# Kernel tuning notes

Measured on AMD Instinct MI355X. Metric: run time of the kernel, lower is better.

The kernel has to match this reference:

```python
import jax, jax.numpy as jnp
import numpy as np

B, N, L, K = 32, 512, 8, 8


def setup_inputs() -> dict:
    key = jax.random.key(0)
    k1, k2 = jax.random.split(key)
    A = jax.random.normal(k1, (B, N, N), dtype=jnp.float32)
    A = 0.5 * (A + A.transpose(0, 2, 1))  # symmetric matrix, as in MMF use-case
    O_stack = jax.random.normal(k2, (L, B, K, K), dtype=jnp.float32)  # per-level KxK rotations
    rng = np.random.default_rng(0)
    idx = np.stack([np.sort(rng.choice(N, K, replace=False)) for _ in range(B * L)])
    indices = jnp.asarray(idx.reshape(B, L, K), dtype=jnp.int32)  # sorted, distinct per (b,l)
    wavelet = indices[:, :, 0]  # wavelet index is one of the selected indices per level
    return {"A": A, "O_stack": O_stack, "indices": indices, "wavelet": wavelet}


def reference(A, O_stack, indices, wavelet):
    Bz, Nz, _ = A.shape
    Lz = O_stack.shape[0]
    eye = jnp.eye(Nz, dtype=A.dtype)

    def build_U(idx, O):
        # identity except the KxK block at (idx_i, idx_j) replaced by O
        # (matches torch boolean-mask row-major fill since idx is sorted)
        return eye.at[idx[:, None], idx[None, :]].set(O)

    right = None
    for l in range(Lz):
        U = jax.vmap(build_U)(indices[:, l], O_stack[l])  # [B,N,N]
        right = U if l == 0 else U @ right
        A = U @ A @ U.transpose(0, 2, 1)

    # final masking: zero rows/cols of wavelet indices, keep diagonal
    active = jnp.ones((Bz, Nz), dtype=A.dtype).at[jnp.arange(Bz)[:, None], wavelet].set(0.0)
    left = active[:, :, None] * active[:, None, :]
    d = jnp.arange(Nz)
    left = left.at[:, d, d].set(1.0)
    D = A * left
    A_rec = right.transpose(0, 2, 1) @ D @ right
    return (A_rec, right, D)
```

## Files before the change

### kernel.cpp

```cpp
#include <hip/hip_runtime.h>

#define BATCH 32
#define NDIM 512
#define LNUM 8
#define KDIM 8

#define WS_PM     0
#define WS_S      512
#define WS_ACT    640
#define WS_W      1152
#define WS_B2     5248
#define WS_C2     9344
#define WS_RA     13440
#define WS_RD     46208
#define WS_RAT    78976
#define WS_RDT    111744
#define WS_STRIDE 144512

#define LSTR 65
typedef float f4 __attribute__((ext_vector_type(4)));

__global__ __launch_bounds__(256) void k_small(
    const float* __restrict__ A, const float* __restrict__ O,
    const int* __restrict__ indices, const int* __restrict__ wavelet,
    float* __restrict__ ws)
{
    const int b = blockIdx.x;
    const int tid = threadIdx.x;
    float* base = ws + (size_t)b * WS_STRIDE;

    __shared__ float Wl[64*LSTR];
    __shared__ float P1[64*LSTR];
    __shared__ float P2[64*LSTR];
    __shared__ float B2l[64*LSTR];
    __shared__ int   pml[NDIM];
    __shared__ float actl[NDIM];
    __shared__ float actS[64];
    __shared__ int   idxsh[64];
    __shared__ int   Ssh[64];
    __shared__ int   prow[KDIM];
    __shared__ float Oall[LNUM*KDIM*KDIM];
    __shared__ int   s_sh;

    for (int t = tid; t < LNUM*KDIM*KDIM; t += 256) {
        int l = t >> 6, k = t & 63;
        Oall[t] = O[((size_t)l*BATCH + b)*(KDIM*KDIM) + k];
    }
    if (tid < 64) idxsh[tid] = indices[b*64 + tid];
    for (int n = tid; n < NDIM; n += 256) { pml[n] = -1; actl[n] = 1.f; }
    __syncthreads();

    if (tid < 64) {
        int n = idxsh[tid];
        bool first = true;
        for (int t = 0; t < tid; ++t) if (idxsh[t] == n) first = false;
        unsigned long long m = __ballot(first);
        int rank = __popcll(m & ((1ull << tid) - 1ull));
        if (first) { pml[n] = rank; Ssh[rank] = n; }
        if (tid == 0) s_sh = (int)__popcll(m);
    }
    if (tid >= 64 && tid < 64 + LNUM) {
        actl[wavelet[b*LNUM + (tid - 64)]] = 0.f;
    }
    __syncthreads();
    const int s = s_sh;
    if (tid < 64 && tid >= s) Ssh[tid] = 0;
    __syncthreads();
    if (tid < 64) actS[tid] = actl[Ssh[tid]];

    {
        int*   g_posmap = (int*)(base + WS_PM);
        int*   g_S      = (int*)(base + WS_S);
        float* g_act    = base + WS_ACT;
        for (int n = tid; n < NDIM; n += 256) { g_posmap[n] = pml[n]; g_act[n] = actl[n]; }
        if (tid < 64) g_S[tid] = Ssh[tid];
    }

    for (int t = tid; t < 4096; t += 256) {
        int rr = t >> 6, cc = t & 63;
        Wl[rr*LSTR + cc] = (rr == cc && rr < s) ? 1.f : 0.f;
    }
    __syncthreads();
    for (int l = 0; l < LNUM; ++l) {
        if (tid < KDIM) prow[tid] = pml[idxsh[l*KDIM + tid]];
        __syncthreads();
        for (int t = tid; t < KDIM*64; t += 256) {
            int i = t >> 6, c = t & 63;
            float acc = 0.f;
            #pragma unroll
            for (int j = 0; j < KDIM; ++j)
                acc += Oall[l*64 + i*KDIM + j] * Wl[prow[j]*LSTR + c];
            B2l[t] = acc;
        }
        __syncthreads();
        for (int t = tid; t < KDIM*64; t += 256) {
            int i = t >> 6, c = t & 63;
            Wl[prow[i]*LSTR + c] = B2l[t];
        }
        __syncthreads();
    }
    {
        float* g_W = base + WS_W;
        for (int t = tid; t < 4096; t += 256) g_W[t] = Wl[(t>>6)*LSTR + (t&63)];
    }

    for (int t = tid; t < 4096; t += 256) {
        int n = t >> 6, m = t & 63;
        P1[n*LSTR + m] = A[((size_t)b*NDIM + Ssh[n])*NDIM + Ssh[m]];
    }
    __syncthreads();

    const int w = tid >> 6;
    const int ln = tid & 63;
    float acc[16];

    #pragma unroll
    for (int k = 0; k < 16; ++k) acc[k] = 0.f;
    for (int n = 0; n < 64; ++n) {
        float as = P1[n*LSTR + ln];
        #pragma unroll
        for (int k = 0; k < 16; ++k) acc[k] += Wl[(w*16 + k)*LSTR + n] * as;
    }
    #pragma unroll
    for (int k = 0; k < 16; ++k) P2[(w*16 + k)*LSTR + ln] = acc[k];
    __syncthreads();

    #pragma unroll
    for (int k = 0; k < 16; ++k) acc[k] = 0.f;
    for (int m = 0; m < 64; ++m) {
        float wv = Wl[ln*LSTR + m];
        #pragma unroll
        for (int k = 0; k < 16; ++k) acc[k] += P2[(w*16 + k)*LSTR + m] * wv;
    }
    #pragma unroll
    for (int k = 0; k < 16; ++k) B2l[(w*16 + k)*LSTR + ln] = acc[k];
    __syncthreads();
    {
        float* g_B2 = base + WS_B2;
        for (int t = tid; t < 4096; t += 256) g_B2[t] = B2l[(t>>6)*LSTR + (t&63)];
    }

    for (int t = tid; t < 4096; t += 256) {
        int n = t >> 6, m = t & 63;
        float mv = (Ssh[n] == Ssh[m]) ? 1.f : actS[n]*actS[m];
        P1[n*LSTR + m] = mv * B2l[n*LSTR + m];
    }
    __syncthreads();

    #pragma unroll
    for (int k = 0; k < 16; ++k) acc[k] = 0.f;
    for (int n = 0; n < 64; ++n) {
        float dv = P1[n*LSTR + ln];
        #pragma unroll
        for (int k = 0; k < 16; ++k) acc[k] += Wl[n*LSTR + (w*16 + k)] * dv;
    }
    #pragma unroll
    for (int k = 0; k < 16; ++k) P2[(w*16 + k)*LSTR + ln] = acc[k];
    __syncthreads();

    #pragma unroll
    for (int k = 0; k < 16; ++k) acc[k] = 0.f;
    for (int m = 0; m < 64; ++m) {
        float wv = Wl[m*LSTR + ln];
        #pragma unroll
        for (int k = 0; k < 16; ++k) acc[k] += P2[(w*16 + k)*LSTR + m] * wv;
    }
    {
        float* g_C2 = base + WS_C2;
        #pragma unroll
        for (int k = 0; k < 16; ++k) g_C2[(w*16 + k)*64 + ln] = acc[k];
    }
}

__global__ __launch_bounds__(256) void k_mid(const float* __restrict__ A,
                                             float* __restrict__ ws)
{
    const int b = blockIdx.x;
    const int j0 = blockIdx.y * 64;
    const int tid = threadIdx.x;
    float* base = ws + (size_t)b * WS_STRIDE;
    const int*   g_S   = (const int*)(base + WS_S);
    const float* g_act = base + WS_ACT;
    const float* g_W   = base + WS_W;
    float* g_RA  = base + WS_RA;
    float* g_RD  = base + WS_RD;
    float* g_RAT = base + WS_RAT;
    float* g_RDT = base + WS_RDT;

    __shared__ float Wl[64*LSTR];
    __shared__ float AS[64*64];
    __shared__ float RAt[64*64];
    __shared__ int   Ssh[64];
    __shared__ float actS[64];
    __shared__ float actj[64];

    for (int t = tid; t < 1024; t += 256) {
        f4 w = ((const f4*)g_W)[t];
        int r = t >> 4, c = (t & 15) * 4;
        Wl[r*LSTR + c]   = w.x; Wl[r*LSTR + c+1] = w.y;
        Wl[r*LSTR + c+2] = w.z; Wl[r*LSTR + c+3] = w.w;
    }
    if (tid < 64) {
        int n = g_S[tid];
        Ssh[tid] = n;
        actS[tid] = g_act[n];
    }
    if (tid >= 64 && tid < 128) actj[tid-64] = g_act[j0 + (tid-64)];
    __syncthreads();

    for (int t = tid; t < 1024; t += 256) {
        int n = t >> 4, cc = (t & 15) * 4;
        f4 v = ((const f4*)(A + ((size_t)b*NDIM + Ssh[n])*NDIM + j0))[t & 15];
        AS[n*64 + cc]   = v.x; AS[n*64 + cc+1] = v.y;
        AS[n*64 + cc+2] = v.z; AS[n*64 + cc+3] = v.w;
    }
    __syncthreads();

    const int g = tid >> 6;
    const int j = tid & 63;
    float racc[16];

    #pragma unroll
    for (int k = 0; k < 16; ++k) racc[k] = 0.f;
    for (int n = 0; n < 64; ++n) {
        float av = AS[n*64 + j];
        #pragma unroll
        for (int k = 0; k < 16; ++k) racc[k] += Wl[(g*16 + k)*LSTR + n] * av;
    }
    #pragma unroll
    for (int k = 0; k < 16; ++k) {
        RAt[(g*16 + k)*64 + j] = racc[k];
        g_RA[(g*16 + k)*NDIM + j0 + j] = racc[k];
    }
    {
        f4* dst = (f4*)(g_RAT + (size_t)(j0 + j)*64 + g*16);
        #pragma unroll
        for (int q = 0; q < 4; ++q) {
            f4 v = { racc[4*q], racc[4*q+1], racc[4*q+2], racc[4*q+3] };
            dst[q] = v;
        }
    }
    __syncthreads();

    #pragma unroll
    for (int k = 0; k < 16; ++k) racc[k] = 0.f;
    for (int n = 0; n < 64; ++n) {
        float dt = actS[n] * RAt[n*64 + j];
        #pragma unroll
        for (int k = 0; k < 16; ++k) racc[k] += Wl[n*LSTR + g*16 + k] * dt;
    }
    const float aj = actj[j];
    #pragma unroll
    for (int k = 0; k < 16; ++k) {
        float rd = racc[k] * aj;
        racc[k] = rd;
        g_RD[(g*16 + k)*NDIM + j0 + j] = rd;
    }
    {
        f4* dst = (f4*)(g_RDT + (size_t)(j0 + j)*64 + g*16);
        #pragma unroll
        for (int q = 0; q < 4; ++q) {
            f4 v = { racc[4*q], racc[4*q+1], racc[4*q+2], racc[4*q+3] };
            dst[q] = v;
        }
    }
}

__global__ __launch_bounds__(256) void k_big(const float* __restrict__ A,
                                             const float* __restrict__ ws,
                                             float* __restrict__ out)
{
    const int b = blockIdx.y;
    const int rh = threadIdx.x >> 7;
    const int lane = threadIdx.x & 127;
    const int i = blockIdx.x*2 + rh;
    const int j0 = lane*4;

    const float* base = ws + (size_t)b * WS_STRIDE;
    const int*   posmap = (const int*)(base + WS_PM);
    const float* act = base + WS_ACT;
    const float* g_W  = base + WS_W;
    const float* g_B2 = base + WS_B2;
    const float* g_C2 = base + WS_C2;
    const float* RA  = base + WS_RA;
    const float* RD  = base + WS_RD;
    const float* RAT = base + WS_RAT;
    const float* RDT = base + WS_RDT;

    const int pi = posmap[i];
    const float acti = act[i];
    const size_t rowoff = ((size_t)b*NDIM + i)*NDIM;
    const size_t seg = (size_t)BATCH*NDIM*NDIM;

    int4   p4  = ((const int4*)posmap)[lane];
    float4 aj4 = ((const float4*)act)[lane];
    int   pm[4] = {p4.x, p4.y, p4.z, p4.w};
    float aj[4] = {aj4.x, aj4.y, aj4.z, aj4.w};

    float a[4], arec[4], dv[4], rv[4];

    if (pi < 0) {
        const float* rat = RAT + (size_t)i*64;
        const float* rdt = RDT + (size_t)i*64;
        float4 v = ((const float4*)(A + rowoff))[lane];
        a[0]=v.x; a[1]=v.y; a[2]=v.z; a[3]=v.w;
        #pragma unroll
        for (int c = 0; c < 4; ++c) {
            int pj = pm[c];
            if (pj >= 0) a[c] = rat[pj];
            float mv = (i == j0 + c) ? 1.f : acti * aj[c];
            dv[c] = a[c] * mv;
            arec[c] = (pj < 0) ? dv[c] : rdt[pj];
            rv[c] = (i == j0 + c) ? 1.f : 0.f;
        }
    } else {
        float4 v = ((const float4*)(RA + (size_t)pi*NDIM))[lane];
        float4 w = ((const float4*)(RD + (size_t)pi*NDIM))[lane];
        a[0]=v.x; a[1]=v.y; a[2]=v.z; a[3]=v.w;
        arec[0]=w.x; arec[1]=w.y; arec[2]=w.z; arec[3]=w.w;
        #pragma unroll
        for (int c = 0; c < 4; ++c) {
            int pj = pm[c];
            if (pj >= 0) {
                a[c]    = g_B2[pi*64 + pj];
                arec[c] = g_C2[pi*64 + pj];
                rv[c]   = g_W[pi*64 + pj];
            } else {
                rv[c] = 0.f;
            }
            float mv = (i == j0 + c) ? 1.f : acti * aj[c];
            dv[c] = a[c] * mv;
        }
    }

    ((float4*)(out + rowoff))[lane]         = make_float4(arec[0], arec[1], arec[2], arec[3]);
    ((float4*)(out + seg + rowoff))[lane]   = make_float4(rv[0], rv[1], rv[2], rv[3]);
    ((float4*)(out + 2*seg + rowoff))[lane] = make_float4(dv[0], dv[1], dv[2], dv[3]);
}

extern "C" void kernel_launch(void* const* d_in, const int* in_sizes, int n_in,
                              void* d_out, int out_size, void* d_ws, size_t ws_size,
                              hipStream_t stream) {
    const float* A       = (const float*)d_in[0];
    const float* O       = (const float*)d_in[1];
    const int*   indices = (const int*)d_in[2];
    const int*   wavelet = (const int*)d_in[3];
    float* ws  = (float*)d_ws;
    float* out = (float*)d_out;

    k_small<<<dim3(BATCH), 256, 0, stream>>>(A, O, indices, wavelet, ws);
    k_mid  <<<dim3(BATCH, 8), 256, 0, stream>>>(A, ws);
    k_big  <<<dim3(NDIM/2, BATCH), 256, 0, stream>>>(A, ws, out);
}
```

Measured before the change: 187.7 us.

## Merge small and mid kernels into one prep launch, add nontemporal IO

Folds k_small and k_mid into a single k_prep grid of (BATCH, 9) blocks. Every block recomputes the cheap W rotation chain. Blocks y<8 then do the per-column-slab RA/RD work, and block y=8 does the small 64x64 B2/C2 products and writes posmap, act and W. This removes one kernel launch and the serial dependency of mid on small, letting the two run concurrently, at the cost of redundant W computation in every block. The big kernel also switches to nontemporal loads of A and nontemporal stores of the three outputs to reduce cache pollution.

After: 178.6 us. 4.9% less time.

```diff
diff --git a/kernel.cpp b/kernel.cpp
--- a/kernel.cpp
+++ b/kernel.cpp
@@ -20,19 +20,20 @@
 #define LSTR 65
 typedef float f4 __attribute__((ext_vector_type(4)));
 
-__global__ __launch_bounds__(256) void k_small(
+__global__ __launch_bounds__(256) void k_prep(
     const float* __restrict__ A, const float* __restrict__ O,
     const int* __restrict__ indices, const int* __restrict__ wavelet,
     float* __restrict__ ws)
 {
-    const int b = blockIdx.x;
+    const int b  = blockIdx.x;
+    const int cy = blockIdx.y;
     const int tid = threadIdx.x;
     float* base = ws + (size_t)b * WS_STRIDE;
 
     __shared__ float Wl[64*LSTR];
-    __shared__ float P1[64*LSTR];
-    __shared__ float P2[64*LSTR];
-    __shared__ float B2l[64*LSTR];
+    __shared__ float Buf1[64*LSTR];
+    __shared__ float Buf2[64*LSTR];
+    __shared__ float Buf3[64*LSTR];
     __shared__ int   pml[NDIM];
     __shared__ float actl[NDIM];
     __shared__ float actS[64];
@@ -68,14 +69,6 @@
     __syncthreads();
     if (tid < 64) actS[tid] = actl[Ssh[tid]];
 
-    {
-        int*   g_posmap = (int*)(base + WS_PM);
-        int*   g_S      = (int*)(base + WS_S);
-        float* g_act    = base + WS_ACT;
-        for (int n = tid; n < NDIM; n += 256) { g_posmap[n] = pml[n]; g_act[n] = actl[n]; }
-        if (tid < 64) g_S[tid] = Ssh[tid];
-    }
-
     for (int t = tid; t < 4096; t += 256) {
         int rr = t >> 6, cc = t & 63;
         Wl[rr*LSTR + cc] = (rr == cc && rr < s) ? 1.f : 0.f;
@@ -90,178 +83,155 @@
             #pragma unroll
             for (int j = 0; j < KDIM; ++j)
                 acc += Oall[l*64 + i*KDIM + j] * Wl[prow[j]*LSTR + c];
-            B2l[t] = acc;
+            Buf3[t] = acc;
         }
         __syncthreads();
         for (int t = tid; t < KDIM*64; t += 256) {
             int i = t >> 6, c = t & 63;
-            Wl[prow[i]*LSTR + c] = B2l[t];
-        }
-        __syncthreads();
-    }
-    {
-        float* g_W = base + WS_W;
-        for (int t = tid; t < 4096; t += 256) g_W[t] = Wl[(t>>6)*LSTR + (t&63)];
-    }
-
-    for (int t = tid; t < 4096; t += 256) {
-        int n = t >> 6, m = t & 63;
-        P1[n*LSTR + m] = A[((size_t)b*NDIM + Ssh[n])*NDIM + Ssh[m]];
-    }
-    __syncthreads();
-
-    const int w = tid >> 6;
-    const int ln = tid & 63;
-    float acc[16];
-
-    #pragma unroll
-    for (int k = 0; k < 16; ++k) acc[k] = 0.f;
-    for (int n = 0; n < 64; ++n) {
-        float as = P1[n*LSTR + ln];
-        #pragma unroll
-        for (int k = 0; k < 16; ++k) acc[k] += Wl[(w*16 + k)*LSTR + n] * as;
-    }
-    #pragma unroll
-    for (int k = 0; k < 16; ++k) P2[(w*16 + k)*LSTR + ln] = acc[k];
-    __syncthreads();
-
-    #pragma unroll
-    for (int k = 0; k < 16; ++k) acc[k] = 0.f;
-    for (int m = 0; m < 64; ++m) {
-        float wv = Wl[ln*LSTR + m];
-        #pragma unroll
-        for (int k = 0; k < 16; ++k) acc[k] += P2[(w*16 + k)*LSTR + m] * wv;
-    }
-    #pragma unroll
-    for (int k = 0; k < 16; ++k) B2l[(w*16 + k)*LSTR + ln] = acc[k];
-    __syncthreads();
-    {
-        float* g_B2 = base + WS_B2;
-        for (int t = tid; t < 4096; t += 256) g_B2[t] = B2l[(t>>6)*LSTR + (t&63)];
-    }
-
-    for (int t = tid; t < 4096; t += 256) {
-        int n = t >> 6, m = t & 63;
-        float mv = (Ssh[n] == Ssh[m]) ? 1.f : actS[n]*actS[m];
-        P1[n*LSTR + m] = mv * B2l[n*LSTR + m];
-    }
-    __syncthreads();
-
-    #pragma unroll
-    for (int k = 0; k < 16; ++k) acc[k] = 0.f;
-    for (int n = 0; n < 64; ++n) {
-        float dv = P1[n*LSTR + ln];
-        #pragma unroll
-        for (int k = 0; k < 16; ++k) acc[k] += Wl[n*LSTR + (w*16 + k)] * dv;
-    }
-    #pragma unroll
-    for (int k = 0; k < 16; ++k) P2[(w*16 + k)*LSTR + ln] = acc[k];
-    __syncthreads();
-
-    #pragma unroll
-    for (int k = 0; k < 16; ++k) acc[k] = 0.f;
-    for (int m = 0; m < 64; ++m) {
-        float wv = Wl[m*LSTR + ln];
-        #pragma unroll
-        for (int k = 0; k < 16; ++k) acc[k] += P2[(w*16 + k)*LSTR + m] * wv;
-    }
-    {
-        float* g_C2 = base + WS_C2;
-        #pragma unroll
-        for (int k = 0; k < 16; ++k) g_C2[(w*16 + k)*64 + ln] = acc[k];
-    }
-}
-
-__global__ __launch_bounds__(256) void k_mid(const float* __restrict__ A,
-                                             float* __restrict__ ws)
-{
-    const int b = blockIdx.x;
-    const int j0 = blockIdx.y * 64;
-    const int tid = threadIdx.x;
-    float* base = ws + (size_t)b * WS_STRIDE;
-    const int*   g_S   = (const int*)(base + WS_S);
-    const float* g_act = base + WS_ACT;
-    const float* g_W   = base + WS_W;
-    float* g_RA  = base + WS_RA;
-    float* g_RD  = base + WS_RD;
-    float* g_RAT = base + WS_RAT;
-    float* g_RDT = base + WS_RDT;
-
-    __shared__ float Wl[64*LSTR];
-    __shared__ float AS[64*64];
-    __shared__ float RAt[64*64];
-    __shared__ int   Ssh[64];
-    __shared__ float actS[64];
-    __shared__ float actj[64];
-
-    for (int t = tid; t < 1024; t += 256) {
-        f4 w = ((const f4*)g_W)[t];
-        int r = t >> 4, c = (t & 15) * 4;
-        Wl[r*LSTR + c]   = w.x; Wl[r*LSTR + c+1] = w.y;
-        Wl[r*LSTR + c+2] = w.z; Wl[r*LSTR + c+3] = w.w;
-    }
-    if (tid < 64) {
-        int n = g_S[tid];
-        Ssh[tid] = n;
-        actS[tid] = g_act[n];
-    }
-    if (tid >= 64 && tid < 128) actj[tid-64] = g_act[j0 + (tid-64)];
-    __syncthreads();
-
-    for (int t = tid; t < 1024; t += 256) {
-        int n = t >> 4, cc = (t & 15) * 4;
-        f4 v = ((const f4*)(A + ((size_t)b*NDIM + Ssh[n])*NDIM + j0))[t & 15];
-        AS[n*64 + cc]   = v.x; AS[n*64 + cc+1] = v.y;
-        AS[n*64 + cc+2] = v.z; AS[n*64 + cc+3] = v.w;
-    }
-    __syncthreads();
-
-    const int g = tid >> 6;
-    const int j = tid & 63;
-    float racc[16];
-
-    #pragma unroll
-    for (int k = 0; k < 16; ++k) racc[k] = 0.f;
-    for (int n = 0; n < 64; ++n) {
-        float av = AS[n*64 + j];
-        #pragma unroll
-        for (int k = 0; k < 16; ++k) racc[k] += Wl[(g*16 + k)*LSTR + n] * av;
-    }
-    #pragma unroll
-    for (int k = 0; k < 16; ++k) {
-        RAt[(g*16 + k)*64 + j] = racc[k];
-        g_RA[(g*16 + k)*NDIM + j0 + j] = racc[k];
-    }
-    {
-        f4* dst = (f4*)(g_RAT + (size_t)(j0 + j)*64 + g*16);
-        #pragma unroll
-        for (int q = 0; q < 4; ++q) {
-            f4 v = { racc[4*q], racc[4*q+1], racc[4*q+2], racc[4*q+3] };
-            dst[q] = v;
-        }
-    }
-    __syncthreads();
-
-    #pragma unroll
-    for (int k = 0; k < 16; ++k) racc[k] = 0.f;
-    for (int n = 0; n < 64; ++n) {
-        float dt = actS[n] * RAt[n*64 + j];
-        #pragma unroll
-        for (int k = 0; k < 16; ++k) racc[k] += Wl[n*LSTR + g*16 + k] * dt;
-    }
-    const float aj = actj[j];
-    #pragma unroll
-    for (int k = 0; k < 16; ++k) {
-        float rd = racc[k] * aj;
-        racc[k] = rd;
-        g_RD[(g*16 + k)*NDIM + j0 + j] = rd;
-    }
-    {
-        f4* dst = (f4*)(g_RDT + (size_t)(j0 + j)*64 + g*16);
-        #pragma unroll
-        for (int q = 0; q < 4; ++q) {
-            f4 v = { racc[4*q], racc[4*q+1], racc[4*q+2], racc[4*q+3] };
-            dst[q] = v;
+            Wl[prow[i]*LSTR + c] = Buf3[t];
+        }
+        __syncthreads();
+    }
+
+    if (cy < 8) {
+        const int j0 = cy * 64;
+        float* AS  = Buf1;
+        float* RAt = Buf2;
+        float* g_RA  = base + WS_RA;
+        float* g_RD  = base + WS_RD;
+        float* g_RAT = base + WS_RAT;
+        float* g_RDT = base + WS_RDT;
+
+        for (int t = tid; t < 1024; t += 256) {
+            int n = t >> 4, cc = (t & 15) * 4;
+            f4 v = ((const f4*)(A + ((size_t)b*NDIM + Ssh[n])*NDIM + j0))[t & 15];
+            AS[n*64 + cc]   = v.x; AS[n*64 + cc+1] = v.y;
+            AS[n*64 + cc+2] = v.z; AS[n*64 + cc+3] = v.w;
+        }
+        __syncthreads();
+
+        const int g = tid >> 6;
+        const int j = tid & 63;
+        float racc[16];
+
+        #pragma unroll
+        for (int k = 0; k < 16; ++k) racc[k] = 0.f;
+        for (int n = 0; n < 64; ++n) {
+            float av = AS[n*64 + j];
+            #pragma unroll
+            for (int k = 0; k < 16; ++k) racc[k] += Wl[(g*16 + k)*LSTR + n] * av;
+        }
+        #pragma unroll
+        for (int k = 0; k < 16; ++k) {
+            RAt[(g*16 + k)*64 + j] = racc[k];
+            g_RA[(g*16 + k)*NDIM + j0 + j] = racc[k];
+        }
+        {
+            f4* dst = (f4*)(g_RAT + (size_t)(j0 + j)*64 + g*16);
+            #pragma unroll
+            for (int q = 0; q < 4; ++q) {
+                f4 v = { racc[4*q], racc[4*q+1], racc[4*q+2], racc[4*q+3] };
+                dst[q] = v;
+            }
+        }
+        __syncthreads();
+
+        #pragma unroll
+        for (int k = 0; k < 16; ++k) racc[k] = 0.f;
+        for (int n = 0; n < 64; ++n) {
+            float dt = actS[n] * RAt[n*64 + j];
+            #pragma unroll
+            for (int k = 0; k < 16; ++k) racc[k] += Wl[n*LSTR + g*16 + k] * dt;
+        }
+        const float aj = actl[j0 + j];
+        #pragma unroll
+        for (int k = 0; k < 16; ++k) {
+            float rd = racc[k] * aj;
+            racc[k] = rd;
+            g_RD[(g*16 + k)*NDIM + j0 + j] = rd;
+        }
+        {
+            f4* dst = (f4*)(g_RDT + (size_t)(j0 + j)*64 + g*16);
+            #pragma unroll
+            for (int q = 0; q < 4; ++q) {
+                f4 v = { racc[4*q], racc[4*q+1], racc[4*q+2], racc[4*q+3] };
+                dst[q] = v;
+            }
+        }
+    } else {
+        {
+            int*   g_posmap = (int*)(base + WS_PM);
+            float* g_act    = base + WS_ACT;
+            float* g_W      = base + WS_W;
+            for (int n = tid; n < NDIM; n += 256) { g_posmap[n] = pml[n]; g_act[n] = actl[n]; }
+            for (int t = tid; t < 4096; t += 256) g_W[t] = Wl[(t>>6)*LSTR + (t&63)];
+        }
+
+        for (int t = tid; t < 4096; t += 256) {
+            int n = t >> 6, m = t & 63;
+            Buf1[n*LSTR + m] = A[((size_t)b*NDIM + Ssh[n])*NDIM + Ssh[m]];
+        }
+        __syncthreads();
+
+        const int w = tid >> 6;
+        const int ln = tid & 63;
+        float acc[16];
+
+        #pragma unroll
+        for (int k = 0; k < 16; ++k) acc[k] = 0.f;
+        for (int n = 0; n < 64; ++n) {
+            float as = Buf1[n*LSTR + ln];
+            #pragma unroll
+            for (int k = 0; k < 16; ++k) acc[k] += Wl[(w*16 + k)*LSTR + n] * as;
+        }
+        #pragma unroll
+        for (int k = 0; k < 16; ++k) Buf2[(w*16 + k)*LSTR + ln] = acc[k];
+        __syncthreads();
+
+        #pragma unroll
+        for (int k = 0; k < 16; ++k) acc[k] = 0.f;
+        for (int m = 0; m < 64; ++m) {
+            float wv = Wl[ln*LSTR + m];
+            #pragma unroll
+            for (int k = 0; k < 16; ++k) acc[k] += Buf2[(w*16 + k)*LSTR + m] * wv;
+        }
+        #pragma unroll
+        for (int k = 0; k < 16; ++k) Buf3[(w*16 + k)*LSTR + ln] = acc[k];
+        __syncthreads();
+        {
+            float* g_B2 = base + WS_B2;
+            for (int t = tid; t < 4096; t += 256) g_B2[t] = Buf3[(t>>6)*LSTR + (t&63)];
+        }
+
+        for (int t = tid; t < 4096; t += 256) {
+            int n = t >> 6, m = t & 63;
+            float mv = (Ssh[n] == Ssh[m]) ? 1.f : actS[n]*actS[m];
+            Buf1[n*LSTR + m] = mv * Buf3[n*LSTR + m];
+        }
+        __syncthreads();
+
+        #pragma unroll
+        for (int k = 0; k < 16; ++k) acc[k] = 0.f;
+        for (int n = 0; n < 64; ++n) {
+            float dv = Buf1[n*LSTR + ln];
+            #pragma unroll
+            for (int k = 0; k < 16; ++k) acc[k] += Wl[n*LSTR + (w*16 + k)] * dv;
+        }
+        #pragma unroll
+        for (int k = 0; k < 16; ++k) Buf2[(w*16 + k)*LSTR + ln] = acc[k];
+        __syncthreads();
+
+        #pragma unroll
+        for (int k = 0; k < 16; ++k) acc[k] = 0.f;
+        for (int m = 0; m < 64; ++m) {
+            float wv = Wl[m*LSTR + ln];
+            #pragma unroll
+            for (int k = 0; k < 16; ++k) acc[k] += Buf2[(w*16 + k)*LSTR + m] * wv;
+        }
+        {
+            float* g_C2 = base + WS_C2;
+            #pragma unroll
+            for (int k = 0; k < 16; ++k) g_C2[(w*16 + k)*64 + ln] = acc[k];
         }
     }
 }
@@ -302,7 +272,7 @@
     if (pi < 0) {
         const float* rat = RAT + (size_t)i*64;
         const float* rdt = RDT + (size_t)i*64;
-        float4 v = ((const float4*)(A + rowoff))[lane];
+        f4 v = __builtin_nontemporal_load((const f4*)(A + rowoff) + lane);
         a[0]=v.x; a[1]=v.y; a[2]=v.z; a[3]=v.w;
         #pragma unroll
         for (int c = 0; c < 4; ++c) {
@@ -314,8 +284,8 @@
             rv[c] = (i == j0 + c) ? 1.f : 0.f;
         }
     } else {
-        float4 v = ((const float4*)(RA + (size_t)pi*NDIM))[lane];
-        float4 w = ((const float4*)(RD + (size_t)pi*NDIM))[lane];
+        f4 v = ((const f4*)(RA + (size_t)pi*NDIM))[lane];
+        f4 w = ((const f4*)(RD + (size_t)pi*NDIM))[lane];
         a[0]=v.x; a[1]=v.y; a[2]=v.z; a[3]=v.w;
         arec[0]=w.x; arec[1]=w.y; arec[2]=w.z; arec[3]=w.w;
         #pragma unroll
@@ -333,9 +303,12 @@
         }
     }
 
-    ((float4*)(out + rowoff))[lane]         = make_float4(arec[0], arec[1], arec[2], arec[3]);
-    ((float4*)(out + seg + rowoff))[lane]   = make_float4(rv[0], rv[1], rv[2], rv[3]);
-    ((float4*)(out + 2*seg + rowoff))[lane] = make_float4(dv[0], dv[1], dv[2], dv[3]);
+    f4 o0; o0.x = arec[0]; o0.y = arec[1]; o0.z = arec[2]; o0.w = arec[3];
+    f4 o1; o1.x = rv[0];   o1.y = rv[1];   o1.z = rv[2];   o1.w = rv[3];
+    f4 o2; o2.x = dv[0];   o2.y = dv[1];   o2.z = dv[2];   o2.w = dv[3];
+    __builtin_nontemporal_store(o0, (f4*)(out + rowoff) + lane);
+    __builtin_nontemporal_store(o1, (f4*)(out + seg + rowoff) + lane);
+    __builtin_nontemporal_store(o2, (f4*)(out + 2*seg + rowoff) + lane);
 }
 
 extern "C" void kernel_launch(void* const* d_in, const int* in_sizes, int n_in,
@@ -348,7 +321,6 @@
     float* ws  = (float*)d_ws;
     float* out = (float*)d_out;
 
-    k_small<<<dim3(BATCH), 256, 0, stream>>>(A, O, indices, wavelet, ws);
-    k_mid  <<<dim3(BATCH, 8), 256, 0, stream>>>(A, ws);
-    k_big  <<<dim3(NDIM/2, BATCH), 256, 0, stream>>>(A, ws, out);
+    k_prep<<<dim3(BATCH, 9), 256, 0, stream>>>(A, O, indices, wavelet, ws);
+    k_big <<<dim3(NDIM/2, BATCH), 256, 0, stream>>>(A, ws, out);
 }
```
